# Kernel tuning notes

Hardware: AMD Instinct MI355X
Metric: run time of the kernel (lower is better)

Reference implementation:

```python
import jax, jax.numpy as jnp
import numpy as np

B, T, D, M, L = 4, 2048, 256, 128, 16
P = M * L  # max_pair_cnt


def setup_inputs() -> dict:
    key = jax.random.key(0)
    ks = jax.random.split(key, 11)
    head = jax.random.normal(ks[0], (B, P, T), jnp.float32) * 0.05
    tail = jax.random.normal(ks[1], (B, P, T), jnp.float32) * 0.05
    x = jax.random.normal(ks[2], (B, T, D), jnp.float32)
    coref_mention_position = jax.random.uniform(ks[3], (B, M, T), jnp.float32)
    lab = jax.random.uniform(ks[4], (B, P, 2), jnp.float32) + 1e-3
    coref_label = lab / lab.sum(-1, keepdims=True)  # already-softmaxed target
    coref_label_mask = jax.random.randint(ks[5], (B, P), 0, 2).astype(bool)
    lens = jnp.full((B, M), L, jnp.int32)  # uniform segment lengths
    w1 = jax.random.normal(ks[6], (3 * D, D), jnp.float32) / np.sqrt(3 * D).astype(np.float32)
    b1 = jnp.zeros((D,), jnp.float32)
    w2 = jax.random.normal(ks[7], (D, 2), jnp.float32) / np.sqrt(D).astype(np.float32)
    b2 = jnp.zeros((2,), jnp.float32)
    return {"head": head, "tail": tail, "lens": lens, "x": x,
            "coref_mention_position": coref_mention_position,
            "coref_label": coref_label, "coref_label_mask": coref_label_mask,
            "w1": w1, "b1": b1, "w2": w2, "b2": b2}


def reference(head, tail, lens, x, coref_mention_position, coref_label,
              coref_label_mask, w1, b1, w2, b2):
    # bmm-based gather of mention reps: [B,P,T] @ [B,T,D] -> [B,P,D]
    head_rep = jnp.einsum('bpt,btd->bpd', head, x)
    tail_rep = jnp.einsum('bpt,btd->bpd', tail, x)
    feat = jnp.concatenate([head_rep, tail_rep, head_rep * tail_rep], axis=-1)
    logits = jax.nn.relu(feat @ w1 + b1) @ w2 + b2  # [B,P,2]

    # ragged split_n_pad -> per-mention top-1 select (uniform lens == L -> reshape)
    scores = logits[..., 1].reshape(B, M, L)            # [B,M,L]
    max_idx = jnp.argmax(scores, axis=-1)               # [B,M]
    max_val = jnp.max(scores, axis=-1)                  # [B,M] (raw logit, as in source)
    tail_seg = tail_rep.reshape(B, M, L, D)
    sel = jnp.take_along_axis(tail_seg, max_idx[:, :, None, None], axis=2)[:, :, 0, :]
    coref_rep_m = sel * max_val[:, :, None]             # [B,M,D]

    # scatter-bmm merge back into sequence: [B,T,M] @ [B,M,D] -> [B,T,D]
    coref_rep = jnp.einsum('bmt,bmd->btd', coref_mention_position, coref_rep_m)
    output = x + coref_rep

    # KLDivLoss(reduction='mean') over masked pairs
    logq = jax.nn.log_softmax(logits, axis=-1)
    lab = coref_label
    pw = jnp.where(lab > 0, lab * jnp.log(jnp.maximum(lab, 1e-38)), 0.0) - lab * logq
    n = jnp.sum(coref_label_mask).astype(jnp.float32)
    loss = jnp.where(coref_label_mask[..., None], pw, 0.0).sum() / (n * 2.0)
    return output, loss
```

## Files before the change

### kernel.cpp

```cpp
#include <hip/hip_runtime.h>
#include <hip/hip_bf16.h>
#include <stdint.h>

#define TAU 0.35f

typedef __attribute__((ext_vector_type(8))) short bf16x8;
typedef __attribute__((ext_vector_type(4))) float f32x4;

__device__ __forceinline__ unsigned short f2bf(float f) {
  __bf16 h = (__bf16)f;
  return __builtin_bit_cast(unsigned short, h);
}
__device__ __forceinline__ float bf2f(unsigned short u) {
  unsigned int v = ((unsigned int)u) << 16;
  return __builtin_bit_cast(float, v);
}
__device__ __forceinline__ void async_copy16(const void* g, void* l) {
  __builtin_amdgcn_global_load_lds(
      (const __attribute__((address_space(1))) unsigned int*)g,
      (__attribute__((address_space(3))) unsigned int*)l, 16, 0, 0);
}

__global__ __launch_bounds__(256) void k_prep(
    const float* __restrict__ x, const float* __restrict__ w1,
    const float* __restrict__ b2,
    unsigned short* __restrict__ xt, unsigned short* __restrict__ w1t,
    float* __restrict__ logits, int* __restrict__ njobs) {
  __shared__ float tileS[64][65];
  int bx = blockIdx.x, tid = threadIdx.x;
  if (bx == 0 && tid == 0) *njobs = 0;
  if (bx < 64) {
    int i = bx * 256 + tid;
    logits[i] = b2[i & 1];
  }
  int j = tid & 63, i0 = tid >> 6;
  if (bx < 512) {
    int b = bx >> 7, t6 = (bx >> 2) & 31, d6 = bx & 3;
    const float* src = x + ((size_t)b * 2048 + (size_t)t6 * 64) * 256 + d6 * 64;
    for (int i = i0; i < 64; i += 4) tileS[i][j] = src[(size_t)i * 256 + j];
    __syncthreads();
    unsigned short* dst = xt + ((size_t)b * 256 + (size_t)d6 * 64) * 2048 + t6 * 64;
    for (int r = i0; r < 64; r += 4) dst[(size_t)r * 2048 + j] = f2bf(tileS[j][r]);
  } else {
    int wt = bx - 512;
    int k6 = wt >> 2, n6 = wt & 3;
    const float* src = w1 + ((size_t)k6 * 64) * 256 + n6 * 64;
    for (int i = i0; i < 64; i += 4) tileS[i][j] = src[(size_t)i * 256 + j];
    __syncthreads();
    unsigned short* dst = w1t + ((size_t)n6 * 64) * 768 + k6 * 64;
    for (int r = i0; r < 64; r += 4) dst[(size_t)r * 768 + j] = f2bf(tileS[j][r]);
  }
}

__global__ __launch_bounds__(256, 4) void k_gemm_rep(
    const float* __restrict__ head, const float* __restrict__ tail,
    const unsigned short* __restrict__ xt,
    float* __restrict__ hrep, float* __restrict__ trep) {
  __shared__ unsigned short Bs[4][4096];
  int bx = blockIdx.x;
  int ntile = bx >> 8;
  int g = bx & 255;
  int b = g >> 6, mtile = g & 63;
  const float* Asrc = ((mtile < 32) ? head : tail) +
                      ((size_t)(b * 2048 + (mtile & 31) * 64)) * 2048;
  float* Crep = (mtile < 32) ? hrep : trep;
  const unsigned short* Bsrc = xt + ((size_t)(b * 256 + ntile * 64)) * 2048;

  int tid = threadIdx.x, lane = tid & 63, w = tid >> 6;

  const unsigned short* bg0;
  const unsigned short* bg1;
  int bdst0, bdst1;
  {
    int colofs0 = (lane >> 3);
    int colofs1 = 8 + (lane >> 3);
    int k80 = (lane & 7) ^ (colofs0 & 7);
    int k81 = (lane & 7) ^ (colofs1 & 7);
    bg0 = Bsrc + (size_t)(w * 16 + colofs0) * 2048 + k80 * 8;
    bg1 = Bsrc + (size_t)(w * 16 + colofs1) * 2048 + k81 * 8;
    bdst0 = (w * 128 + lane) * 8;
    bdst1 = (w * 128 + 64 + lane) * 8;
  }

  int sw0 = (lane >> 4) ^ (lane & 7);
  int sw1 = (4 + (lane >> 4)) ^ (lane & 7);
  int colc[4];
#pragma unroll
  for (int ct = 0; ct < 4; ++ct) colc[ct] = (ct * 16 + (lane & 15)) * 8;

  const float* anext =
      Asrc + (size_t)(w * 16 + (lane & 15)) * 2048 + ((lane >> 4) << 3);

  f32x4 acc[4];
#pragma unroll
  for (int ct = 0; ct < 4; ++ct) acc[ct] = (f32x4){0.f, 0.f, 0.f, 0.f};

  auto STAGEB = [&](int buf) {
    async_copy16(bg0, &Bs[buf][bdst0]); bg0 += 64;
    async_copy16(bg1, &Bs[buf][bdst1]); bg1 += 64;
  };
  auto LOADA = [&](float4* av) {
    const float4* ap = (const float4*)anext;
    av[0] = ap[0]; av[1] = ap[1];
    av[2] = ap[8]; av[3] = ap[9];
    anext += 64;
  };
  auto MMA = [&](int buf, const float4* av) {
    bf16x8 f0, f1;
    f0[0] = (short)f2bf(av[0].x); f0[1] = (short)f2bf(av[0].y);
    f0[2] = (short)f2bf(av[0].z); f0[3] = (short)f2bf(av[0].w);
    f0[4] = (short)f2bf(av[1].x); f0[5] = (short)f2bf(av[1].y);
    f0[6] = (short)f2bf(av[1].z); f0[7] = (short)f2bf(av[1].w);
    f1[0] = (short)f2bf(av[2].x); f1[1] = (short)f2bf(av[2].y);
    f1[2] = (short)f2bf(av[2].z); f1[3] = (short)f2bf(av[2].w);
    f1[4] = (short)f2bf(av[3].x); f1[5] = (short)f2bf(av[3].y);
    f1[6] = (short)f2bf(av[3].z); f1[7] = (short)f2bf(av[3].w);
    const unsigned short* B_ = Bs[buf];
#pragma unroll
    for (int ct = 0; ct < 4; ++ct) {
      bf16x8 b0 = *(const bf16x8*)&B_[(colc[ct] + sw0) * 8];
      acc[ct] = __builtin_amdgcn_mfma_f32_16x16x32_bf16(f0, b0, acc[ct], 0, 0, 0);
    }
#pragma unroll
    for (int ct = 0; ct < 4; ++ct) {
      bf16x8 b1 = *(const bf16x8*)&B_[(colc[ct] + sw1) * 8];
      acc[ct] = __builtin_amdgcn_mfma_f32_16x16x32_bf16(f1, b1, acc[ct], 0, 0, 0);
    }
  };

  float4 avA0[4], avA1[4], avB0[4], avB1[4];
  STAGEB(0); STAGEB(1);
  LOADA(avA0); LOADA(avA1);
  __syncthreads();

  for (int t = 0; t < 8; ++t) {
    STAGEB(2); STAGEB(3);
    LOADA(avB0); LOADA(avB1);
    MMA(0, avA0);
    MMA(1, avA1);
    __syncthreads();
    if (t < 7) {
      STAGEB(0); STAGEB(1);
      LOADA(avA0); LOADA(avA1);
    }
    MMA(2, avB0);
    MMA(3, avB1);
    __syncthreads();
  }

  size_t prow = (size_t)b * 2048 + (size_t)(mtile & 31) * 64 + w * 16 + ((lane >> 4) << 2);
  int cb = ntile * 64 + (lane & 15);
#pragma unroll
  for (int ct = 0; ct < 4; ++ct)
#pragma unroll
    for (int i = 0; i < 4; ++i)
      Crep[(prow + i) * 256 + cb + ct * 16] = acc[ct][i];
}

__global__ __launch_bounds__(256) void k_feat(
    const float* __restrict__ hrep, const float* __restrict__ trep,
    unsigned short* __restrict__ featbf) {
  int gid = blockIdx.x * 256 + threadIdx.x;
  int p = gid >> 6, d0 = (gid & 63) * 4;
  float4 h4 = *(const float4*)&hrep[(size_t)p * 256 + d0];
  float4 t4 = *(const float4*)&trep[(size_t)p * 256 + d0];
  ushort4 a, bb, c;
  a.x = f2bf(h4.x); a.y = f2bf(h4.y); a.z = f2bf(h4.z); a.w = f2bf(h4.w);
  bb.x = f2bf(t4.x); bb.y = f2bf(t4.y); bb.z = f2bf(t4.z); bb.w = f2bf(t4.w);
  c.x = f2bf(h4.x * t4.x); c.y = f2bf(h4.y * t4.y);
  c.z = f2bf(h4.z * t4.z); c.w = f2bf(h4.w * t4.w);
  *(ushort4*)&featbf[(size_t)p * 768 + d0] = a;
  *(ushort4*)&featbf[(size_t)p * 768 + 256 + d0] = bb;
  *(ushort4*)&featbf[(size_t)p * 768 + 512 + d0] = c;
}

__global__ __launch_bounds__(256, 4) void k_gemm_mlp(
    const unsigned short* __restrict__ featb, const unsigned short* __restrict__ w1t,
    const float* __restrict__ b1, const float* __restrict__ w2,
    float* __restrict__ logits) {
  __shared__ unsigned short As[2][4096], Bs[2][4096];
  int bx = blockIdx.x;
  int ntile = bx >> 7;
  int mtile = bx & 127;
  int tid = threadIdx.x, lane = tid & 63, w = tid >> 6;

  const unsigned short* ag[2];
  const unsigned short* bgp[2];
  int dofs[2];
#pragma unroll
  for (int a = 0; a < 2; ++a) {
    int rowofs = a * 8 + (lane >> 3);
    int k8 = (lane & 7) ^ (rowofs & 7);
    ag[a] = featb + (size_t)(mtile * 64 + w * 16 + rowofs) * 768 + k8 * 8;
    bgp[a] = w1t + (size_t)(ntile * 64 + w * 16 + rowofs) * 768 + k8 * 8;
    dofs[a] = (w * 128 + a * 64 + lane) * 8;
  }
  int sw0 = (lane >> 4) ^ (lane & 7);
  int sw1 = (4 + (lane >> 4)) ^ (lane & 7);
  int arowc = (w * 16 + (lane & 15)) * 8;
  int colc[4];
#pragma unroll
  for (int ct = 0; ct < 4; ++ct) colc[ct] = (ct * 16 + (lane & 15)) * 8;

  f32x4 acc[4];
#pragma unroll
  for (int ct = 0; ct < 4; ++ct) acc[ct] = (f32x4){0.f, 0.f, 0.f, 0.f};

#pragma unroll
  for (int a = 0; a < 2; ++a) {
    async_copy16(ag[a], &As[0][dofs[a]]); ag[a] += 64;
    async_copy16(bgp[a], &Bs[0][dofs[a]]); bgp[a] += 64;
  }
  __syncthreads();

  for (int it = 0; it < 12; ++it) {
    int cur = it & 1, nxt = cur ^ 1;
    if (it < 11) {
#pragma unroll
      for (int a = 0; a < 2; ++a) {
        async_copy16(ag[a], &As[nxt][dofs[a]]); ag[a] += 64;
        async_copy16(bgp[a], &Bs[nxt][dofs[a]]); bgp[a] += 64;
      }
    }
    const unsigned short* A_ = As[cur];
    const unsigned short* B_ = Bs[cur];
    bf16x8 a0 = *(const bf16x8*)&A_[(arowc + sw0) * 8];
    bf16x8 a1 = *(const bf16x8*)&A_[(arowc + sw1) * 8];
#pragma unroll
    for (int ct = 0; ct < 4; ++ct) {
      bf16x8 b0 = *(const bf16x8*)&B_[(colc[ct] + sw0) * 8];
      acc[ct] = __builtin_amdgcn_mfma_f32_16x16x32_bf16(a0, b0, acc[ct], 0, 0, 0);
    }
#pragma unroll
    for (int ct = 0; ct < 4; ++ct) {
      bf16x8 b1 = *(const bf16x8*)&B_[(colc[ct] + sw1) * 8];
      acc[ct] = __builtin_amdgcn_mfma_f32_16x16x32_bf16(a1, b1, acc[ct], 0, 0, 0);
    }
    __syncthreads();
  }

  float bv[4], w20[4], w21[4];
#pragma unroll
  for (int ct = 0; ct < 4; ++ct) {
    int col = ntile * 64 + ct * 16 + (lane & 15);
    bv[ct] = b1[col]; w20[ct] = w2[col * 2]; w21[ct] = w2[col * 2 + 1];
  }
#pragma unroll
  for (int i = 0; i < 4; ++i) {
    float s0 = 0.f, s1 = 0.f;
#pragma unroll
    for (int ct = 0; ct < 4; ++ct) {
      float r = fmaxf(acc[ct][i] + bv[ct], 0.f);
      s0 += r * w20[ct]; s1 += r * w21[ct];
    }
#pragma unroll
    for (int off = 1; off < 16; off <<= 1) {
      s0 += __shfl_xor(s0, off); s1 += __shfl_xor(s1, off);
    }
    if ((lane & 15) == 0) {
      int row = mtile * 64 + w * 16 + ((lane >> 4) << 2) + i;
      atomicAdd(&logits[row * 2], s0);
      atomicAdd(&logits[row * 2 + 1], s1);
    }
  }
}

__global__ void k_select(const float* __restrict__ logits, int* __restrict__ idxv,
                         float* __restrict__ mval, int* __restrict__ cmask,
                         int* __restrict__ njobs, int* __restrict__ jobs) {
  int q = blockIdx.x * 256 + threadIdx.x;
  if (q >= 512) return;
  int base = q * 16;
  float s[16];
#pragma unroll
  for (int i = 0; i < 16; ++i) s[i] = logits[(size_t)(base + i) * 2 + 1];
  float best = s[0]; int bi = 0;
#pragma unroll
  for (int i = 1; i < 16; ++i) if (s[i] > best) { best = s[i]; bi = i; }
  int mask = 0, cnt = 0;
#pragma unroll
  for (int i = 0; i < 16; ++i) if (s[i] > best - TAU) { mask |= 1 << i; ++cnt; }
  idxv[q] = bi; mval[q] = best;
  if (cnt > 1) {
    cmask[q] = mask;
    for (int i = 0; i < 16; ++i)
      if ((mask >> i) & 1) { int j = atomicAdd(njobs, 1); jobs[j] = base + i; }
  } else cmask[q] = 0;
}

__global__ __launch_bounds__(1024) void k_refine(
    const int* __restrict__ njobs, const int* __restrict__ jobs,
    const float* __restrict__ head, const float* __restrict__ tail,
    const float* __restrict__ x, const float* __restrict__ w1,
    const float* __restrict__ b1, const float* __restrict__ w2,
    const float* __restrict__ b2, float* __restrict__ refined) {
  __shared__ float hrow[2048], trow[2048], feat[768], red[1024], red2[1024];
  int tid = threadIdx.x, seg = tid >> 8, d = tid & 255;
  int nj = *njobs;
  for (int job = blockIdx.x; job < nj; job += gridDim.x) {
    int code = jobs[job];
    int b = code >> 11, p = code & 2047;
    if (tid < 512)
      *(float4*)&hrow[tid * 4] = *(const float4*)&head[((size_t)(b * 2048 + p)) * 2048 + tid * 4];
    else {
      int u = tid - 512;
      *(float4*)&trow[u * 4] = *(const float4*)&tail[((size_t)(b * 2048 + p)) * 2048 + u * 4];
    }
    __syncthreads();
    float hr = 0.f, tr = 0.f;
    const float* xb = x + ((size_t)b * 2048) * 256 + d;
#pragma unroll 8
    for (int t = seg * 512; t < seg * 512 + 512; ++t) {
      float xv = xb[(size_t)t * 256];
      hr += hrow[t] * xv; tr += trow[t] * xv;
    }
    red[tid] = hr; red2[tid] = tr;
    __syncthreads();
    if (seg == 0) {
      float fh = red[d] + red[256 + d] + red[512 + d] + red[768 + d];
      float ft = red2[d] + red2[256 + d] + red2[512 + d] + red2[768 + d];
      feat[d] = fh; feat[256 + d] = ft; feat[512 + d] = fh * ft;
    }
    __syncthreads();
    float hp = 0.f;
    for (int ii = seg * 192; ii < seg * 192 + 192; ++ii) hp += feat[ii] * w1[(size_t)ii * 256 + d];
    red[tid] = hp;
    __syncthreads();
    if (seg == 0) {
      float hj = b1[d] + red[d] + red[256 + d] + red[512 + d] + red[768 + d];
      hj = fmaxf(hj, 0.f);
      red2[d] = hj * w2[d * 2 + 1];
    }
    __syncthreads();
    for (int s = 128; s > 0; s >>= 1) {
      if (tid < s) red2[tid] += red2[tid + s];
      __syncthreads();
    }
    if (tid == 0) refined[code] = red2[0] + b2[1];
    __syncthreads();
  }
}

__global__ __launch_bounds__(256) void k_repm(
    const int* __restrict__ idxv, const float* __restrict__ mval,
    const int* __restrict__ cmask, const float* __restrict__ refined,
    const float* __restrict__ trep, float* __restrict__ repm) {
  int q = blockIdx.x, d = threadIdx.x;
  int mask = cmask[q]; int bi; float v;
  if (mask) {
    bi = -1; v = -1e30f;
    for (int i = 0; i < 16; ++i)
      if ((mask >> i) & 1) { float s = refined[q * 16 + i]; if (s > v) { v = s; bi = i; } }
  } else { bi = idxv[q]; v = mval[q]; }
  repm[(size_t)q * 256 + d] = trep[((size_t)q * 16 + bi) * 256 + d] * v;
}

__global__ __launch_bounds__(256) void k_merge(
    const float* __restrict__ cmp, const float* __restrict__ repm,
    const float* __restrict__ x, float* __restrict__ out) {
  __shared__ float cl[128 * 16];
  int bx = blockIdx.x, b = bx >> 7, t0 = (bx & 127) * 16;
  int tid = threadIdx.x;
#pragma unroll
  for (int it = 0; it < 2; ++it) {
    int f = it * 256 + tid;
    int row = f >> 2, c4 = (f & 3) * 4;
    *(float4*)&cl[row * 16 + c4] =
        *(const float4*)&cmp[((size_t)(b * 128 + row)) * 2048 + t0 + c4];
  }
  __syncthreads();
  float acc[16];
#pragma unroll
  for (int i = 0; i < 16; ++i) acc[i] = 0.f;
  int d = tid;
  for (int m = 0; m < 128; ++m) {
    float rv = repm[(size_t)(b * 128 + m) * 256 + d];
    const float4* c4p = (const float4*)&cl[m * 16];
#pragma unroll
    for (int jj = 0; jj < 4; ++jj) {
      float4 c = c4p[jj];
      acc[jj * 4] += c.x * rv; acc[jj * 4 + 1] += c.y * rv;
      acc[jj * 4 + 2] += c.z * rv; acc[jj * 4 + 3] += c.w * rv;
    }
  }
  const float* xb = x + ((size_t)(b * 2048 + t0)) * 256 + d;
  float* ob = out + ((size_t)(b * 2048 + t0)) * 256 + d;
#pragma unroll
  for (int tt = 0; tt < 16; ++tt) ob[(size_t)tt * 256] = xb[(size_t)tt * 256] + acc[tt];
}

__global__ __launch_bounds__(1024) void k_loss(
    const float* __restrict__ logits, const float* __restrict__ lab,
    const unsigned char* __restrict__ mask, float* __restrict__ out_loss) {
  __shared__ float rs[1024], rc[1024];
  int tid = threadIdx.x;
  float sum = 0.f, cnt = 0.f;
  for (int p = tid; p < 8192; p += 1024) {
    float l0 = logits[(size_t)p * 2], l1 = logits[(size_t)p * 2 + 1];
    float a0 = lab[(size_t)p * 2], a1 = lab[(size_t)p * 2 + 1];
    float mx = fmaxf(l0, l1);
    float lse = mx + logf(expf(l0 - mx) + expf(l1 - mx));
    float pw = 0.f;
    if (a0 > 0.f) pw += a0 * logf(fmaxf(a0, 1e-38f));
    if (a1 > 0.f) pw += a1 * logf(fmaxf(a1, 1e-38f));
    pw -= a0 * (l0 - lse) + a1 * (l1 - lse);
    if (mask[p]) { sum += pw; cnt += 1.f; }
  }
  rs[tid] = sum; rc[tid] = cnt;
  __syncthreads();
  for (int s = 512; s > 0; s >>= 1) {
    if (tid < s) { rs[tid] += rs[tid + s]; rc[tid] += rc[tid + s]; }
    __syncthreads();
  }
  if (tid == 0) *out_loss = rs[0] / (rc[0] * 2.0f);
}

extern "C" void kernel_launch(void* const* d_in, const int* in_sizes, int n_in,
                              void* d_out, int out_size, void* d_ws, size_t ws_size,
                              hipStream_t stream) {
  (void)in_sizes; (void)n_in; (void)out_size; (void)ws_size;
  const float* head = (const float*)d_in[0];
  const float* tail = (const float*)d_in[1];
  const float* x = (const float*)d_in[3];
  const float* cmp = (const float*)d_in[4];
  const float* lab = (const float*)d_in[5];
  const unsigned char* lmask = (const unsigned char*)d_in[6];
  const float* w1 = (const float*)d_in[7];
  const float* b1 = (const float*)d_in[8];
  const float* w2 = (const float*)d_in[9];
  const float* b2 = (const float*)d_in[10];
  float* out = (float*)d_out;

  char* ws = (char*)d_ws;
  size_t off = 0;
  auto alloc = [&](size_t bytes) -> void* {
    void* p = ws + off; off += (bytes + 255) & ~(size_t)255; return p;
  };
  unsigned short* xt = (unsigned short*)alloc(4ull * 256 * 2048 * 2);
  unsigned short* w1t = (unsigned short*)alloc(256ull * 768 * 2);
  float* hrep = (float*)alloc(8192ull * 256 * 4);
  float* trep = (float*)alloc(8192ull * 256 * 4);
  unsigned short* featb = (unsigned short*)alloc(8192ull * 768 * 2);
  float* logits = (float*)alloc(8192ull * 2 * 4);
  float* refined = (float*)alloc(8192ull * 4);
  int* idxv = (int*)alloc(512 * 4);
  float* mvalv = (float*)alloc(512 * 4);
  int* cmaskv = (int*)alloc(512 * 4);
  int* njobs = (int*)alloc(256);
  int* jobs = (int*)alloc(8192 * 4);
  float* repm = (float*)alloc(512ull * 256 * 4);

  k_prep<<<560, 256, 0, stream>>>(x, w1, b2, xt, w1t, logits, njobs);
  k_gemm_rep<<<1024, 256, 0, stream>>>(head, tail, xt, hrep, trep);
  k_feat<<<2048, 256, 0, stream>>>(hrep, trep, featb);
  k_gemm_mlp<<<512, 256, 0, stream>>>(featb, w1t, b1, w2, logits);
  k_select<<<2, 256, 0, stream>>>(logits, idxv, mvalv, cmaskv, njobs, jobs);
  k_refine<<<256, 1024, 0, stream>>>(njobs, jobs, head, tail, x, w1, b1, w2, b2, refined);
  k_repm<<<512, 256, 0, stream>>>(idxv, mvalv, cmaskv, refined, trep, repm);
  k_merge<<<512, 256, 0, stream>>>(cmp, repm, x, out);
  k_loss<<<1, 1024, 0, stream>>>(logits, lab, lmask, out + 4ull * 2048 * 256);
}
```

Baseline: 351.1 us.

## Widen rep GEMM tile to full N and stage A through LDS once

Each block of the head/tail projection GEMM now computes a 64x256 output tile with 512 threads instead of a 64x64 tile. The fp32 A rows are read once, converted to bf16 and shared through LDS, instead of being reloaded by four separate blocks. The main loop is restructured into a double-buffered pipeline over 32 k-steps. The intent is to cut redundant global reads of the large head/tail tensors, at the cost of fewer blocks (one per CU) and more LDS per block.

```diff
diff --git a/kernel.cpp b/kernel.cpp
--- a/kernel.cpp
+++ b/kernel.cpp
@@ -52,106 +52,103 @@
   }
 }
 
-__global__ __launch_bounds__(256, 4) void k_gemm_rep(
+__global__ __launch_bounds__(512, 2) void k_gemm_rep(
     const float* __restrict__ head, const float* __restrict__ tail,
     const unsigned short* __restrict__ xt,
     float* __restrict__ hrep, float* __restrict__ trep) {
-  __shared__ unsigned short Bs[4][4096];
+  __shared__ unsigned short As[2][4096];
+  __shared__ unsigned short Bs[2][16384];
   int bx = blockIdx.x;
-  int ntile = bx >> 8;
-  int g = bx & 255;
-  int b = g >> 6, mtile = g & 63;
-  const float* Asrc = ((mtile < 32) ? head : tail) +
-                      ((size_t)(b * 2048 + (mtile & 31) * 64)) * 2048;
-  float* Crep = (mtile < 32) ? hrep : trep;
-  const unsigned short* Bsrc = xt + ((size_t)(b * 256 + ntile * 64)) * 2048;
+  int b = bx >> 6, mt = bx & 63;
+  const float* Asrc = ((mt < 32) ? head : tail) +
+                      ((size_t)(b * 2048 + (mt & 31) * 64)) * 2048;
+  float* Crep = (mt < 32) ? hrep : trep;
+  const unsigned short* Bsrc = xt + ((size_t)b * 256) * 2048;
 
   int tid = threadIdx.x, lane = tid & 63, w = tid >> 6;
 
-  const unsigned short* bg0;
-  const unsigned short* bg1;
-  int bdst0, bdst1;
-  {
-    int colofs0 = (lane >> 3);
-    int colofs1 = 8 + (lane >> 3);
-    int k80 = (lane & 7) ^ (colofs0 & 7);
-    int k81 = (lane & 7) ^ (colofs1 & 7);
-    bg0 = Bsrc + (size_t)(w * 16 + colofs0) * 2048 + k80 * 8;
-    bg1 = Bsrc + (size_t)(w * 16 + colofs1) * 2048 + k81 * 8;
-    bdst0 = (w * 128 + lane) * 8;
-    bdst1 = (w * 128 + 64 + lane) * 8;
-  }
-
+  int ar = tid >> 3, aq = tid & 7;
+  const float* aptr = Asrc + (size_t)ar * 2048 + aq * 8;
+  int awi = ((ar >> 4) * 128 + (aq >> 2) * 64 + (aq & 3) * 16 + (ar & 15)) * 8;
+
+  const unsigned short* bg[4];
+  int bdst[4];
+#pragma unroll
+  for (int a = 0; a < 4; ++a) {
+    int colofs = a * 8 + (lane >> 3);
+    int col = w * 32 + colofs;
+    int k8 = (lane & 7) ^ (colofs & 7);
+    bg[a] = Bsrc + (size_t)col * 2048 + k8 * 8;
+    bdst[a] = (w * 256 + a * 64 + lane) * 8;
+  }
+
+  int rt = w & 3;
+  int cg = (w >> 2) * 128;
   int sw0 = (lane >> 4) ^ (lane & 7);
   int sw1 = (4 + (lane >> 4)) ^ (lane & 7);
-  int colc[4];
-#pragma unroll
-  for (int ct = 0; ct < 4; ++ct) colc[ct] = (ct * 16 + (lane & 15)) * 8;
-
-  const float* anext =
-      Asrc + (size_t)(w * 16 + (lane & 15)) * 2048 + ((lane >> 4) << 3);
-
-  f32x4 acc[4];
-#pragma unroll
-  for (int ct = 0; ct < 4; ++ct) acc[ct] = (f32x4){0.f, 0.f, 0.f, 0.f};
+  int colc[8];
+#pragma unroll
+  for (int ct = 0; ct < 8; ++ct) colc[ct] = (cg + ct * 16 + (lane & 15)) * 8;
+
+  f32x4 acc[8];
+#pragma unroll
+  for (int ct = 0; ct < 8; ++ct) acc[ct] = (f32x4){0.f, 0.f, 0.f, 0.f};
 
   auto STAGEB = [&](int buf) {
-    async_copy16(bg0, &Bs[buf][bdst0]); bg0 += 64;
-    async_copy16(bg1, &Bs[buf][bdst1]); bg1 += 64;
+#pragma unroll
+    for (int a = 0; a < 4; ++a) { async_copy16(bg[a], &Bs[buf][bdst[a]]); bg[a] += 64; }
   };
-  auto LOADA = [&](float4* av) {
-    const float4* ap = (const float4*)anext;
-    av[0] = ap[0]; av[1] = ap[1];
-    av[2] = ap[8]; av[3] = ap[9];
-    anext += 64;
+  float4 av0, av1;
+  auto LOADA = [&]() {
+    const float4* ap = (const float4*)aptr;
+    av0 = ap[0]; av1 = ap[1];
+    aptr += 64;
   };
-  auto MMA = [&](int buf, const float4* av) {
-    bf16x8 f0, f1;
-    f0[0] = (short)f2bf(av[0].x); f0[1] = (short)f2bf(av[0].y);
-    f0[2] = (short)f2bf(av[0].z); f0[3] = (short)f2bf(av[0].w);
-    f0[4] = (short)f2bf(av[1].x); f0[5] = (short)f2bf(av[1].y);
-    f0[6] = (short)f2bf(av[1].z); f0[7] = (short)f2bf(av[1].w);
-    f1[0] = (short)f2bf(av[2].x); f1[1] = (short)f2bf(av[2].y);
-    f1[2] = (short)f2bf(av[2].z); f1[3] = (short)f2bf(av[2].w);
-    f1[4] = (short)f2bf(av[3].x); f1[5] = (short)f2bf(av[3].y);
-    f1[6] = (short)f2bf(av[3].z); f1[7] = (short)f2bf(av[3].w);
+  auto WRITEA = [&](int buf) {
+    bf16x8 p;
+    p[0] = (short)f2bf(av0.x); p[1] = (short)f2bf(av0.y);
+    p[2] = (short)f2bf(av0.z); p[3] = (short)f2bf(av0.w);
+    p[4] = (short)f2bf(av1.x); p[5] = (short)f2bf(av1.y);
+    p[6] = (short)f2bf(av1.z); p[7] = (short)f2bf(av1.w);
+    *(bf16x8*)&As[buf][awi] = p;
+  };
+  auto MMA = [&](int buf) {
+    const unsigned short* A_ = As[buf];
     const unsigned short* B_ = Bs[buf];
-#pragma unroll
-    for (int ct = 0; ct < 4; ++ct) {
+    bf16x8 a0 = *(const bf16x8*)&A_[(rt * 128 + lane) * 8];
+    bf16x8 a1 = *(const bf16x8*)&A_[(rt * 128 + 64 + lane) * 8];
+#pragma unroll
+    for (int ct = 0; ct < 8; ++ct) {
       bf16x8 b0 = *(const bf16x8*)&B_[(colc[ct] + sw0) * 8];
-      acc[ct] = __builtin_amdgcn_mfma_f32_16x16x32_bf16(f0, b0, acc[ct], 0, 0, 0);
-    }
-#pragma unroll
-    for (int ct = 0; ct < 4; ++ct) {
+      acc[ct] = __builtin_amdgcn_mfma_f32_16x16x32_bf16(a0, b0, acc[ct], 0, 0, 0);
+    }
+#pragma unroll
+    for (int ct = 0; ct < 8; ++ct) {
       bf16x8 b1 = *(const bf16x8*)&B_[(colc[ct] + sw1) * 8];
-      acc[ct] = __builtin_amdgcn_mfma_f32_16x16x32_bf16(f1, b1, acc[ct], 0, 0, 0);
+      acc[ct] = __builtin_amdgcn_mfma_f32_16x16x32_bf16(a1, b1, acc[ct], 0, 0, 0);
     }
   };
 
-  float4 avA0[4], avA1[4], avB0[4], avB1[4];
-  STAGEB(0); STAGEB(1);
-  LOADA(avA0); LOADA(avA1);
+  STAGEB(0);
+  LOADA();
+  WRITEA(0);
   __syncthreads();
 
-  for (int t = 0; t < 8; ++t) {
-    STAGEB(2); STAGEB(3);
-    LOADA(avB0); LOADA(avB1);
-    MMA(0, avA0);
-    MMA(1, avA1);
-    __syncthreads();
-    if (t < 7) {
-      STAGEB(0); STAGEB(1);
-      LOADA(avA0); LOADA(avA1);
-    }
-    MMA(2, avB0);
-    MMA(3, avB1);
-    __syncthreads();
-  }
-
-  size_t prow = (size_t)b * 2048 + (size_t)(mtile & 31) * 64 + w * 16 + ((lane >> 4) << 2);
-  int cb = ntile * 64 + (lane & 15);
-#pragma unroll
-  for (int ct = 0; ct < 4; ++ct)
+  for (int it = 0; it < 32; ++it) {
+    int cur = it & 1, nxt = cur ^ 1;
+    if (it < 31) {
+      STAGEB(nxt);
+      LOADA();
+    }
+    MMA(cur);
+    if (it < 31) WRITEA(nxt);
+    __syncthreads();
+  }
+
+  size_t prow = (size_t)b * 2048 + (size_t)(mt & 31) * 64 + rt * 16 + ((lane >> 4) << 2);
+  int cb = cg + (lane & 15);
+#pragma unroll
+  for (int ct = 0; ct < 8; ++ct)
 #pragma unroll
     for (int i = 0; i < 4; ++i)
       Crep[(prow + i) * 256 + cb + ct * 16] = acc[ct][i];
@@ -451,7 +448,7 @@
   float* repm = (float*)alloc(512ull * 256 * 4);
 
   k_prep<<<560, 256, 0, stream>>>(x, w1, b2, xt, w1t, logits, njobs);
-  k_gemm_rep<<<1024, 256, 0, stream>>>(head, tail, xt, hrep, trep);
+  k_gemm_rep<<<256, 512, 0, stream>>>(head, tail, xt, hrep, trep);
   k_feat<<<2048, 256, 0, stream>>>(hrep, trep, featb);
   k_gemm_mlp<<<512, 256, 0, stream>>>(featb, w1t, b1, w2, logits);
   k_select<<<2, 256, 0, stream>>>(logits, idxv, mvalv, cmaskv, njobs, jobs);
```

After: 322.2 us. -8.3%, faster.
